# Kernel tuning notes

Hardware: AMD Instinct MI355X
Metric: run time of the kernel (lower is better)

## Reference

```python
import jax, jax.numpy as jnp
import numpy as np


def _make_stencil():
    # Fixed finite-difference kernels from the torch module __init__
    w = np.zeros((4, 1, 3, 3), np.float32)
    w[0, 0, 1, 1] = 1.0; w[0, 0, 1, 2] = -1.0   # self - right
    w[1, 0, 1, 0] = 1.0; w[1, 0, 1, 1] = -1.0   # left - self
    w[2, 0, 1, 1] = 1.0; w[2, 0, 2, 1] = -1.0   # self - down
    w[3, 0, 0, 1] = 1.0; w[3, 0, 1, 1] = -1.0   # up - self
    return jnp.asarray(w)


def setup_inputs() -> dict:
    key = jax.random.key(0)
    H, W, S = 2160, 3840, 512
    seg = jax.random.randint(key, (1, 1, H, W), 0, S, dtype=jnp.int32)
    return {"seg": seg, "w": _make_stencil(), "num_segments": S}


def reference(seg, w, num_segments):
    S = int(num_segments)
    H, W_ = seg.shape[2], seg.shape[3]
    x = seg.astype(jnp.float32)
    # Conv2d(padding=3, padding_mode='replicate'): edge-pad by 3 then VALID 3x3 conv
    xp = jnp.pad(x, ((0, 0), (0, 0), (3, 3), (3, 3)), mode='edge')
    res = jax.lax.conv_general_dilated(
        xp, w, window_strides=(1, 1), padding='VALID',
        dimension_numbers=('NCHW', 'OIHW', 'NCHW'))  # (1,4,H+4,W+4)
    bm = (res != 0)[0, :, 2:-2, 2:-2]  # (4,H,W); boundary masks per direction

    s2 = seg[0, 0]  # (H,W) int
    # In the torch code, the k-th True of mask0 at (y,x) pairs with the k-th True
    # of mask1 at (y,x+1) (mask1 is mask0 shifted by +1 in x; replicate padding
    # guarantees equal counts). Hence horizontal edges are (seg[y,x], seg[y,x+1])
    # where bm[0], and vertical edges (seg[y,x], seg[y+1,x]) where bm[2].
    right_nb = jnp.concatenate([s2[:, 1:], s2[:, -1:]], axis=1)
    down_nb = jnp.concatenate([s2[1:, :], s2[-1:, :]], axis=0)

    flat = s2.ravel()
    adj = jnp.zeros((S, S), jnp.float32)
    adj = adj.at[flat, right_nb.ravel()].add(bm[0].astype(jnp.float32).ravel())
    adj = adj.at[flat, down_nb.ravel()].add(bm[2].astype(jnp.float32).ravel())
    # unique pairs -> presence matrix; diagonal (self-pairs) never occurs in original
    adj = jnp.where(adj > 0, 1.0, 0.0) * (1.0 - jnp.eye(S, dtype=jnp.float32))

    # centers(): per-segment mean of (x_index, y_index) -- the torch permute
    # reverses dims so column 0 is the W-axis mean, column 1 the H-axis mean.
    ys = jnp.broadcast_to(jnp.arange(H, dtype=jnp.float32)[:, None], (H, W_)).ravel()
    xs = jnp.broadcast_to(jnp.arange(W_, dtype=jnp.float32)[None, :], (H, W_)).ravel()
    cnt = jax.ops.segment_sum(jnp.ones_like(xs), flat, num_segments=S)
    sx = jax.ops.segment_sum(xs, flat, num_segments=S)
    sy = jax.ops.segment_sum(ys, flat, num_segments=S)
    centers = jnp.stack([sx, sy], axis=1) / cnt[:, None]
    return adj, centers
```

## Files before the change

kernel.cpp:

```cpp
#include <hip/hip_runtime.h>

#define HH 2160
#define WW 3840
#define SS 512
#define NWORDS (SS * SS / 32)

typedef unsigned int uint;
typedef unsigned long long ull;

__global__ __launch_bounds__(512) void seg_main(
    const int* __restrict__ seg, uint* __restrict__ wsOr,
    uint* __restrict__ part, int nb) {
  __shared__ uint s_bm[NWORDS];
  __shared__ ull  s_pk[SS];
  __shared__ uint s_sx[SS];
  for (int i = threadIdx.x; i < NWORDS; i += blockDim.x) s_bm[i] = 0u;
  for (int i = threadIdx.x; i < SS; i += blockDim.x) { s_pk[i] = 0ULL; s_sx[i] = 0u; }
  __syncthreads();

  const int NC = HH * WW / 4;
  const int stride = gridDim.x * blockDim.x;
  const int4* __restrict__ seg4  = (const int4*)seg;
  const int4* __restrict__ seg4d = (const int4*)(seg + WW);

  for (int c = blockIdx.x * blockDim.x + threadIdx.x; c < NC; c += stride) {
    const int p = c * 4;
    const int y = p / WW;
    const int x = p - y * WW;
    const int4 v = seg4[c];
    const int4 d = (y < HH - 1) ? seg4d[c] : v;
    const int nxt = (x < WW - 4) ? seg[p + 4] : v.w;

    if (v.x != v.y) { int i = v.x * SS + v.y; atomicOr(&s_bm[i >> 5], 1u << (i & 31)); }
    if (v.y != v.z) { int i = v.y * SS + v.z; atomicOr(&s_bm[i >> 5], 1u << (i & 31)); }
    if (v.z != v.w) { int i = v.z * SS + v.w; atomicOr(&s_bm[i >> 5], 1u << (i & 31)); }
    if (v.w != nxt) { int i = v.w * SS + nxt; atomicOr(&s_bm[i >> 5], 1u << (i & 31)); }
    if (v.x != d.x) { int i = v.x * SS + d.x; atomicOr(&s_bm[i >> 5], 1u << (i & 31)); }
    if (v.y != d.y) { int i = v.y * SS + d.y; atomicOr(&s_bm[i >> 5], 1u << (i & 31)); }
    if (v.z != d.z) { int i = v.z * SS + d.z; atomicOr(&s_bm[i >> 5], 1u << (i & 31)); }
    if (v.w != d.w) { int i = v.w * SS + d.w; atomicOr(&s_bm[i >> 5], 1u << (i & 31)); }

    const ull yp = (1ULL << 40) | (ull)(uint)y;
    atomicAdd(&s_pk[v.x], yp); atomicAdd(&s_sx[v.x], (uint)x);
    atomicAdd(&s_pk[v.y], yp); atomicAdd(&s_sx[v.y], (uint)(x + 1));
    atomicAdd(&s_pk[v.z], yp); atomicAdd(&s_sx[v.z], (uint)(x + 2));
    atomicAdd(&s_pk[v.w], yp); atomicAdd(&s_sx[v.w], (uint)(x + 3));
  }
  __syncthreads();

  for (int i = threadIdx.x; i < NWORDS; i += blockDim.x) {
    const uint val = s_bm[i];
    if (val) atomicOr(&wsOr[i], val);
  }
  for (int i = threadIdx.x; i < SS; i += blockDim.x) {
    const ull pk = s_pk[i];
    part[(0 * SS + i) * nb + blockIdx.x] = (uint)(pk >> 40);
    part[(1 * SS + i) * nb + blockIdx.x] = s_sx[i];
    part[(2 * SS + i) * nb + blockIdx.x] = (uint)(pk & ((1ULL << 40) - 1));
  }
}

__global__ __launch_bounds__(256) void adj_expand(
    const uint* __restrict__ wsOr, float* __restrict__ adj) {
  const int t = blockIdx.x * 256 + threadIdx.x;
  const uint bits = (wsOr[t >> 3] >> ((t & 7) * 4)) & 0xFu;
  float4 q;
  q.x = (bits & 1u) ? 1.0f : 0.0f;
  q.y = (bits & 2u) ? 1.0f : 0.0f;
  q.z = (bits & 4u) ? 1.0f : 0.0f;
  q.w = (bits & 8u) ? 1.0f : 0.0f;
  ((float4*)adj)[t] = q;
}

__global__ __launch_bounds__(64) void seg_reduce(
    const uint* __restrict__ part, int nb, float* __restrict__ centers) {
  const int s = blockIdx.x;
  const int t = threadIdx.x;
  ull cnt = 0, sx = 0, sy = 0;
  for (int b = t; b < nb; b += 64) {
    cnt += part[(0 * SS + s) * nb + b];
    sx  += part[(1 * SS + s) * nb + b];
    sy  += part[(2 * SS + s) * nb + b];
  }
  for (int off = 32; off > 0; off >>= 1) {
    cnt += __shfl_down(cnt, off, 64);
    sx  += __shfl_down(sx,  off, 64);
    sy  += __shfl_down(sy,  off, 64);
  }
  if (t == 0) {
    const double dc = (double)cnt;
    centers[s * 2 + 0] = (float)((double)sx / dc);
    centers[s * 2 + 1] = (float)((double)sy / dc);
  }
}

extern "C" void kernel_launch(void* const* d_in, const int* in_sizes, int n_in,
                              void* d_out, int out_size, void* d_ws, size_t ws_size,
                              hipStream_t stream) {
  const int* seg = (const int*)d_in[0];
  float* out = (float*)d_out;
  float* adj = out;
  float* centers = out + SS * SS;

  uint* wsOr = (uint*)d_ws;
  uint* part = wsOr + NWORDS;

  int nb = 512;
  const size_t fixed = (size_t)NWORDS * sizeof(uint);
  const size_t per_block = (size_t)SS * 3 * sizeof(uint);
  if (ws_size < fixed + (size_t)nb * per_block) {
    nb = (int)((ws_size - fixed) / per_block);
    if (nb > 512) nb = 512;
    if (nb < 1) nb = 1;
  }

  hipMemsetAsync(wsOr, 0, fixed, stream);
  seg_main<<<nb, 512, 0, stream>>>(seg, wsOr, part, nb);
  adj_expand<<<SS * SS / 4 / 256, 256, 0, stream>>>(wsOr, adj);
  seg_reduce<<<SS, 64, 0, stream>>>(part, nb, centers);
}
```

Measured before the change: 112.1 us.

## Replace global atomicOr bitmap merge with per-block bitmaps and fused finalize kernel

Each block now writes its full shared-memory adjacency bitmap to a private workspace slice instead of issuing global atomicOr on non-zero words. This also removes the memset. A single finalize kernel OR-reduces the per-block bitmaps row by row, expands them to floats, and computes the centers in the same launch. That cuts two launches and the global atomic contention, but each block now writes 32 KB and the finalize pass reads up to 16 MB of bitmaps.

```diff
diff --git a/kernel.cpp b/kernel.cpp
--- a/kernel.cpp
+++ b/kernel.cpp
@@ -3,18 +3,19 @@
 #define HH 2160
 #define WW 3840
 #define SS 512
-#define NWORDS (SS * SS / 32)
+#define NW (SS * SS / 32)
+#define NBMAX 512
 
 typedef unsigned int uint;
 typedef unsigned long long ull;
 
 __global__ __launch_bounds__(512) void seg_main(
-    const int* __restrict__ seg, uint* __restrict__ wsOr,
+    const int* __restrict__ seg, uint* __restrict__ wsBm,
     uint* __restrict__ part, int nb) {
-  __shared__ uint s_bm[NWORDS];
+  __shared__ uint s_bm[NW];
   __shared__ ull  s_pk[SS];
   __shared__ uint s_sx[SS];
-  for (int i = threadIdx.x; i < NWORDS; i += blockDim.x) s_bm[i] = 0u;
+  for (int i = threadIdx.x; i < NW; i += blockDim.x) s_bm[i] = 0u;
   for (int i = threadIdx.x; i < SS; i += blockDim.x) { s_pk[i] = 0ULL; s_sx[i] = 0u; }
   __syncthreads();
 
@@ -48,10 +49,9 @@
   }
   __syncthreads();
 
-  for (int i = threadIdx.x; i < NWORDS; i += blockDim.x) {
-    const uint val = s_bm[i];
-    if (val) atomicOr(&wsOr[i], val);
-  }
+  uint* myBm = wsBm + (size_t)blockIdx.x * NW;
+  for (int i = threadIdx.x; i < NW; i += blockDim.x) myBm[i] = s_bm[i];
+
   for (int i = threadIdx.x; i < SS; i += blockDim.x) {
     const ull pk = s_pk[i];
     part[(0 * SS + i) * nb + blockIdx.x] = (uint)(pk >> 40);
@@ -60,37 +60,57 @@
   }
 }
 
-__global__ __launch_bounds__(256) void adj_expand(
-    const uint* __restrict__ wsOr, float* __restrict__ adj) {
-  const int t = blockIdx.x * 256 + threadIdx.x;
-  const uint bits = (wsOr[t >> 3] >> ((t & 7) * 4)) & 0xFu;
-  float4 q;
-  q.x = (bits & 1u) ? 1.0f : 0.0f;
-  q.y = (bits & 2u) ? 1.0f : 0.0f;
-  q.z = (bits & 4u) ? 1.0f : 0.0f;
-  q.w = (bits & 8u) ? 1.0f : 0.0f;
-  ((float4*)adj)[t] = q;
-}
+__global__ __launch_bounds__(256) void finalize(
+    const uint* __restrict__ wsBm, const uint* __restrict__ part, int nb,
+    float* __restrict__ adj, float* __restrict__ centers) {
+  const int g = blockIdx.x;
+  const int t = threadIdx.x;
 
-__global__ __launch_bounds__(64) void seg_reduce(
-    const uint* __restrict__ part, int nb, float* __restrict__ centers) {
-  const int s = blockIdx.x;
-  const int t = threadIdx.x;
-  ull cnt = 0, sx = 0, sy = 0;
-  for (int b = t; b < nb; b += 64) {
-    cnt += part[(0 * SS + s) * nb + b];
-    sx  += part[(1 * SS + s) * nb + b];
-    sy  += part[(2 * SS + s) * nb + b];
-  }
-  for (int off = 32; off > 0; off >>= 1) {
-    cnt += __shfl_down(cnt, off, 64);
-    sx  += __shfl_down(sx,  off, 64);
-    sy  += __shfl_down(sy,  off, 64);
-  }
-  if (t == 0) {
-    const double dc = (double)cnt;
-    centers[s * 2 + 0] = (float)((double)sx / dc);
-    centers[s * 2 + 1] = (float)((double)sy / dc);
+  if (g < SS) {
+    const int k  = t & 15;
+    const int bg = t >> 4;
+    uint acc = 0u;
+    const uint* base = wsBm + g * 16 + k;
+    for (int b = bg; b < nb; b += 16) acc |= base[(size_t)b * NW];
+
+    __shared__ uint s_red[16][16];
+    __shared__ uint s_word[16];
+    s_red[bg][k] = acc;
+    __syncthreads();
+    if (t < 16) {
+      uint w = 0u;
+      #pragma unroll
+      for (int i = 0; i < 16; i++) w |= s_red[i][t];
+      s_word[t] = w;
+    }
+    __syncthreads();
+    if (t < 128) {
+      const int cell = t * 4;
+      const uint nib = (s_word[cell >> 5] >> (cell & 31)) & 0xFu;
+      float4 q;
+      q.x = (nib & 1u) ? 1.0f : 0.0f;
+      q.y = (nib & 2u) ? 1.0f : 0.0f;
+      q.z = (nib & 4u) ? 1.0f : 0.0f;
+      q.w = (nib & 8u) ? 1.0f : 0.0f;
+      ((float4*)(adj + g * SS))[t] = q;
+    }
+  } else {
+    const int s = (g - SS) * 64 + (t >> 2);
+    const int q = t & 3;
+    ull cnt = 0, sx = 0, sy = 0;
+    for (int b = q; b < nb; b += 4) {
+      cnt += part[(0 * SS + s) * nb + b];
+      sx  += part[(1 * SS + s) * nb + b];
+      sy  += part[(2 * SS + s) * nb + b];
+    }
+    cnt += __shfl_down(cnt, 2, 4); cnt += __shfl_down(cnt, 1, 4);
+    sx  += __shfl_down(sx,  2, 4); sx  += __shfl_down(sx,  1, 4);
+    sy  += __shfl_down(sy,  2, 4); sy  += __shfl_down(sy,  1, 4);
+    if (q == 0) {
+      const double dc = (double)cnt;
+      centers[s * 2 + 0] = (float)((double)sx / dc);
+      centers[s * 2 + 1] = (float)((double)sy / dc);
+    }
   }
 }
 
@@ -102,20 +122,16 @@
   float* adj = out;
   float* centers = out + SS * SS;
 
-  uint* wsOr = (uint*)d_ws;
-  uint* part = wsOr + NWORDS;
-
-  int nb = 512;
-  const size_t fixed = (size_t)NWORDS * sizeof(uint);
-  const size_t per_block = (size_t)SS * 3 * sizeof(uint);
-  if (ws_size < fixed + (size_t)nb * per_block) {
-    nb = (int)((ws_size - fixed) / per_block);
-    if (nb > 512) nb = 512;
+  int nb = NBMAX;
+  const size_t per_block = (size_t)(NW + 3 * SS) * sizeof(uint);
+  if (ws_size < (size_t)nb * per_block) {
+    nb = (int)(ws_size / per_block);
+    if (nb > NBMAX) nb = NBMAX;
     if (nb < 1) nb = 1;
   }
+  uint* wsBm = (uint*)d_ws;
+  uint* part = wsBm + (size_t)nb * NW;
 
-  hipMemsetAsync(wsOr, 0, fixed, stream);
-  seg_main<<<nb, 512, 0, stream>>>(seg, wsOr, part, nb);
-  adj_expand<<<SS * SS / 4 / 256, 256, 0, stream>>>(wsOr, adj);
-  seg_reduce<<<SS, 64, 0, stream>>>(part, nb, centers);
+  seg_main<<<nb, 512, 0, stream>>>(seg, wsBm, part, nb);
+  finalize<<<SS + 8, 256, 0, stream>>>(wsBm, part, nb, adj, centers);
 }
```

Result: slower. 124.9 us (+11.5%).
